# Performance work log

Hardware: AMD Instinct MI355X
Metric: run time of the kernel (lower is better)

The kernel has to match this reference:

```python
import jax, jax.numpy as jnp
import numpy as np

CHUNK = 16
GROUPS = 8
EPS = 1e-5


def setup_inputs() -> dict:
    key = jax.random.key(0)
    ks = jax.random.split(key, 8)
    B, C, H, W = 8, 1, 2048, 2048
    D_in = C * CHUNK * CHUNK  # 256
    D = 16                    # out_channels
    x = jax.random.normal(ks[0], (B, C, H, W), dtype=jnp.float32)
    s_fc = 1.0 / np.sqrt(D_in)
    fc_wr = jax.random.normal(ks[1], (D, D_in), dtype=jnp.float32) * s_fc
    fc_wi = jax.random.normal(ks[2], (D, D_in), dtype=jnp.float32) * s_fc
    fc_br = jax.random.normal(ks[3], (D,), dtype=jnp.float32) * s_fc
    fc_bi = jax.random.normal(ks[4], (D,), dtype=jnp.float32) * s_fc
    conv_w = jax.random.normal(ks[5], (D, D), dtype=jnp.float32) * (1.0 / np.sqrt(D))
    conv_b = jax.random.normal(ks[6], (D,), dtype=jnp.float32) * 0.05
    gamma = jnp.ones((D,), dtype=jnp.float32)
    beta = jnp.zeros((D,), dtype=jnp.float32)
    return {"x": x, "fc_wr": fc_wr, "fc_wi": fc_wi, "fc_br": fc_br,
            "fc_bi": fc_bi, "conv_w": conv_w, "conv_b": conv_b,
            "gamma": gamma, "beta": beta}


def reference(x, fc_wr, fc_wi, fc_br, fc_bi, conv_w, conv_b, gamma, beta):
    B, C, H, W = x.shape
    s = CHUNK
    h, w = H // s, W // s
    D = fc_wr.shape[0]
    # rearrange 'b c (h s1) (w s2) -> (b h w) (s1 s2 c)'
    p = x.reshape(B, C, h, s, w, s)
    p = p.transpose(0, 2, 4, 3, 5, 1).reshape(B * h * w, s * s * C)
    # FFT over the flattened patch dim (ortho norm) -> complex64
    fft = jnp.fft.fft(p, norm="ortho")
    Wc = fc_wr + 1j * fc_wi           # [D, D_in] complex
    bc = fc_br + 1j * fc_bi           # [D]
    fc = fft @ Wc.T + bc              # [N, D] complex linear
    # IFFT over channel dim (size D), keep real part
    y = jnp.fft.ifft(fc, norm="ortho").real  # [N, D] float32
    # '(b h w) d -> b d h w'
    y = y.reshape(B, h, w, D).transpose(0, 3, 1, 2)
    # 1x1 conv
    y = jnp.einsum("bdhw,ed->behw", y, conv_w) + conv_b[None, :, None, None]
    # GroupNorm(GROUPS, D)
    yg = y.reshape(B, GROUPS, D // GROUPS, h, w)
    mean = yg.mean(axis=(2, 3, 4), keepdims=True)
    var = yg.var(axis=(2, 3, 4), keepdims=True)
    yn = ((yg - mean) * jax.lax.rsqrt(var + EPS)).reshape(B, D, h, w)
    return yn * gamma[None, :, None, None] + beta[None, :, None, None]
```

## Files before the change

### kernel.cpp

```cpp
#include <hip/hip_runtime.h>
#include <math.h>

#define PI_F 3.14159265358979323846f


#define WS_AH    0
#define WS_U     2048
#define WS_STATS 2112

using half8   = __attribute__((ext_vector_type(8))) _Float16;
using floatx4 = __attribute__((ext_vector_type(4))) float;

__device__ __forceinline__ void gload_lds16(const void* g, void* l) {
    __builtin_amdgcn_global_load_lds(
        (const __attribute__((address_space(1))) uint32_t*)g,
        (__attribute__((address_space(3))) uint32_t*)l,
        16, 0, 0);
}

__global__ __launch_bounds__(256) void prep(
        const float* __restrict__ wr, const float* __restrict__ wi,
        const float* __restrict__ br, const float* __restrict__ bi,
        const float* __restrict__ cw, const float* __restrict__ cb,
        float* __restrict__ ws) {
    const int e = blockIdx.x;
    const int t = threadIdx.x;
    __shared__ float c16[16], s16[16], Fr[16], Fi[16];
    __shared__ float Gr[256], Gi[256], cosT[256], sinT[256];

    float ang = (2.0f * PI_F / 256.0f) * (float)t;
    cosT[t] = cosf(ang);
    sinT[t] = sinf(ang);
    if (t < 16) {
        float a = (2.0f * PI_F / 16.0f) * (float)t;
        c16[t] = cosf(a);
        s16[t] = sinf(a);
    }
    __syncthreads();

    if (t < 16) {
        float fr = 0.f, fi = 0.f;
        #pragma unroll
        for (int m = 0; m < 16; ++m) {
            float c = cw[e * 16 + m];
            fr += c * c16[(t * m) & 15];
            fi += c * s16[(t * m) & 15];
        }
        Fr[t] = fr;
        Fi[t] = fi;
    }
    __syncthreads();

    {
        float gr = 0.f, gi = 0.f;
        #pragma unroll
        for (int d = 0; d < 16; ++d) {
            float wrv = wr[d * 256 + t];
            float wiv = wi[d * 256 + t];
            gr += wrv * Fr[d] - wiv * Fi[d];
            gi += wrv * Fi[d] + wiv * Fr[d];
        }
        Gr[t] = gr;
        Gi[t] = gi;
    }
    if (t == 0) {
        float s = 0.f;
        #pragma unroll
        for (int d = 0; d < 16; ++d) s += br[d] * Fr[d] - bi[d] * Fi[d];
        ws[WS_U + e] = cb[e] + 0.25f * s;
    }
    __syncthreads();

    float acc = 0.f;
    for (int k = 0; k < 256; ++k) {
        int a = (k * t) & 255;
        acc += Gr[k] * cosT[a] + Gi[k] * sinT[a];
    }
    _Float16* Ah = (_Float16*)(ws + WS_AH);
    Ah[e * 256 + t] = (_Float16)(acc * (1.0f / 64.0f));

    if (e == 0 && t < 128) ws[WS_STATS + t] = 0.f;
}

__global__ __launch_bounds__(256) void main_k(const float* __restrict__ x,
                                              const float* __restrict__ ws,
                                              float* __restrict__ out,
                                              float* __restrict__ stats) {
    __shared__ float x_sh[4 * 4096];
    __shared__ float s_sum[4][8], s_ssq[4][8];
    const int t = threadIdx.x;

    const int w    = t >> 6;
    const int lane = t & 63;
    const int m    = lane & 15;
    const int kg   = lane >> 4;
    const int r_off = (kg >> 1);
    const int c_off = (kg & 1) << 3;

    const _Float16* Ah = (const _Float16*)(ws + WS_AH);
    half8 Areg[8];
    #pragma unroll
    for (int s = 0; s < 8; ++s)
        Areg[s] = *(const half8*)(Ah + m * 256 + s * 32 + kg * 8);
    const float u = ws[WS_U + m];

    const int P0  = blockIdx.x << 6;
    const int b   = P0 >> 14;
    const int pi  = P0 & 16383;
    const int ph  = pi >> 7;
    const int pw0 = pi & 127;

    const float* xb = x + ((size_t)b << 22)
                        + (size_t)(ph << 4) * 2048
                        + (size_t)((pw0 + w * 16 + m) << 4);

    float* lp = x_sh + w * 4096;
    #pragma unroll
    for (int j = 0; j < 16; ++j) {
        const int s = j >> 1, h = j & 1;
        const float* src = xb + (size_t)(2 * s + r_off) * 2048 + c_off + 4 * h;
        gload_lds16(src, lp + j * 256);
    }

    floatx4 acc = {0.f, 0.f, 0.f, 0.f};
    const float* xw = x_sh + w * 4096 + lane * 4;

#define WAITVM(N) asm volatile("s_waitcnt vmcnt(" #N ")" ::: "memory")
#define STEP(S, VM) do {                                                 \
        WAITVM(VM);                                                      \
        const float4 c0 = *(const float4*)(xw + (S) * 512);              \
        const float4 c1 = *(const float4*)(xw + (S) * 512 + 256);        \
        half8 a;                                                         \
        a[0] = (_Float16)c0.x; a[1] = (_Float16)c0.y;                    \
        a[2] = (_Float16)c0.z; a[3] = (_Float16)c0.w;                    \
        a[4] = (_Float16)c1.x; a[5] = (_Float16)c1.y;                    \
        a[6] = (_Float16)c1.z; a[7] = (_Float16)c1.w;                    \
        acc = __builtin_amdgcn_mfma_f32_16x16x32_f16(a, Areg[S], acc,    \
                                                     0, 0, 0);           \
    } while (0)

    STEP(0, 14);
    STEP(1, 12);
    STEP(2, 10);
    STEP(3, 8);
    STEP(4, 6);
    STEP(5, 4);
    STEP(6, 2);
    STEP(7, 0);
#undef STEP
#undef WAITVM

    float v0 = acc[0] + u;
    float v1 = acc[1] + u;
    float v2 = acc[2] + u;
    float v3 = acc[3] + u;
    *(float4*)&out[((size_t)b << 18) + (size_t)m * 16384
                   + (size_t)(ph << 7) + (size_t)(pw0 + w * 16 + kg * 4)]
        = make_float4(v0, v1, v2, v3);

    float sv = v0 + v1 + v2 + v3;
    float qv = v0 * v0 + v1 * v1 + v2 * v2 + v3 * v3;
    sv += __shfl_xor(sv, 16, 64);  qv += __shfl_xor(qv, 16, 64);
    sv += __shfl_xor(sv, 32, 64);  qv += __shfl_xor(qv, 32, 64);
    sv += __shfl_xor(sv, 1, 64);   qv += __shfl_xor(qv, 1, 64);
    if (kg == 0 && (m & 1) == 0) {
        s_sum[w][m >> 1] = sv;
        s_ssq[w][m >> 1] = qv;
    }
    __syncthreads();
    if (t < 8) {
        float S = s_sum[0][t] + s_sum[1][t] + s_sum[2][t] + s_sum[3][t];
        float Q = s_ssq[0][t] + s_ssq[1][t] + s_ssq[2][t] + s_ssq[3][t];
        atomicAdd(&stats[b * 8 + t],      S);
        atomicAdd(&stats[64 + b * 8 + t], Q);
    }
}

__global__ __launch_bounds__(256) void finalize(float* __restrict__ out,
                                                const float* __restrict__ stats,
                                                const float* __restrict__ gamma,
                                                const float* __restrict__ beta) {
    const int i    = blockIdx.x * 256 + threadIdx.x;
    const int flat = i << 2;
    const int b = flat >> 18;
    const int c = (flat >> 14) & 15;
    const int g = c >> 1;

    const float inv_n = 1.0f / 32768.0f;
    float mean = stats[b * 8 + g] * inv_n;
    float var  = stats[64 + b * 8 + g] * inv_n - mean * mean;
    float rstd = rsqrtf(var + 1e-5f);
    float sc = rstd * gamma[c];
    float sh = beta[c] - mean * sc;

    float4 vv = ((float4*)out)[i];
    vv.x = vv.x * sc + sh;
    vv.y = vv.y * sc + sh;
    vv.z = vv.z * sc + sh;
    vv.w = vv.w * sc + sh;
    ((float4*)out)[i] = vv;
}

extern "C" void kernel_launch(void* const* d_in, const int* in_sizes, int n_in,
                              void* d_out, int out_size, void* d_ws, size_t ws_size,
                              hipStream_t stream) {
    const float* x  = (const float*)d_in[0];
    const float* wr = (const float*)d_in[1];
    const float* wi = (const float*)d_in[2];
    const float* br = (const float*)d_in[3];
    const float* bi = (const float*)d_in[4];
    const float* cw = (const float*)d_in[5];
    const float* cb = (const float*)d_in[6];
    const float* gm = (const float*)d_in[7];
    const float* bt = (const float*)d_in[8];
    float* out = (float*)d_out;
    float* ws  = (float*)d_ws;

    prep<<<16, 256, 0, stream>>>(wr, wi, br, bi, cw, cb, ws);
    main_k<<<2048, 256, 0, stream>>>(x, ws, out, ws + WS_STATS);
    finalize<<<2048, 256, 0, stream>>>(out, ws + WS_STATS, gm, bt);
}
```

Measured before the change: 220.2 us.

## Fuse GroupNorm finalize into main kernel via cooperative grid sync

Replaces the separate finalize pass with a cooperative launch of 512 blocks, each processing four patch tiles with double-buffered global-to-LDS loads. After the grid-wide sync the blocks read the group statistics and write normalized outputs straight from registers. This avoids writing and re-reading the full output tensor and drops one kernel launch. In exchange it relies on all 512 blocks being co-resident and adds grid-sync latency and less parallelism per block.

```diff
diff --git a/kernel.cpp b/kernel.cpp
--- a/kernel.cpp
+++ b/kernel.cpp
@@ -1,5 +1,8 @@
 #include <hip/hip_runtime.h>
+#include <hip/hip_cooperative_groups.h>
 #include <math.h>
+
+namespace cg = cooperative_groups;
 
 #define PI_F 3.14159265358979323846f
 
@@ -85,8 +88,10 @@
 __global__ __launch_bounds__(256) void main_k(const float* __restrict__ x,
                                               const float* __restrict__ ws,
                                               float* __restrict__ out,
+                                              const float* __restrict__ gamma,
+                                              const float* __restrict__ beta,
                                               float* __restrict__ stats) {
-    __shared__ float x_sh[4 * 4096];
+    __shared__ float x_sh[16384];
     __shared__ float s_sum[4][8], s_ssq[4][8];
     const int t = threadIdx.x;
 
@@ -104,62 +109,89 @@
         Areg[s] = *(const half8*)(Ah + m * 256 + s * 32 + kg * 8);
     const float u = ws[WS_U + m];
 
-    const int P0  = blockIdx.x << 6;
-    const int b   = P0 >> 14;
-    const int pi  = P0 & 16383;
-    const int ph  = pi >> 7;
-    const int pw0 = pi & 127;
-
-    const float* xb = x + ((size_t)b << 22)
-                        + (size_t)(ph << 4) * 2048
-                        + (size_t)((pw0 + w * 16 + m) << 4);
-
-    float* lp = x_sh + w * 4096;
-    #pragma unroll
-    for (int j = 0; j < 16; ++j) {
-        const int s = j >> 1, h = j & 1;
-        const float* src = xb + (size_t)(2 * s + r_off) * 2048 + c_off + 4 * h;
-        gload_lds16(src, lp + j * 256);
-    }
-
+    const int T0  = blockIdx.x << 2;
+    const int b   = T0 >> 8;
+    const int tb0 = T0 & 255;
+    const int ph01 = tb0 >> 1;
+    const int cl   = (w * 16 + m) << 4;
+
+    const float* xB  = x + ((size_t)b << 22);
+    const float* xbA = xB + (size_t)(ph01 << 4) * 2048 + cl;
+    const float* xbB = xbA + 1024;
+    const float* xbC = xbA + 32768;
+    const float* xbD = xbC + 1024;
+
+#define ISSUE(G, XB) do {                                                  \
+        float* lp_ = x_sh + ((G) & 1) * 8192 + w * 2048;                   \
+        _Pragma("unroll")                                                  \
+        for (int j = 0; j < 8; ++j) {                                      \
+            const int sg_ = ((G) & 1) * 4 + (j >> 1);                      \
+            const float* src_ = (XB) + (size_t)(2 * sg_ + r_off) * 2048    \
+                                + c_off + 4 * (j & 1);                     \
+            gload_lds16(src_, lp_ + j * 256);                              \
+        }                                                                  \
+    } while (0)
+
+    const float* xw0 = x_sh + w * 2048 + lane * 4;
+    const float* xw1 = xw0 + 8192;
+
+#define STEP(BUFP, SL, SG, VMLIT) do {                                     \
+        asm volatile("s_waitcnt vmcnt(" #VMLIT ")" ::: "memory");          \
+        const float4 c0 = *(const float4*)((BUFP) + (SL) * 512);           \
+        const float4 c1 = *(const float4*)((BUFP) + (SL) * 512 + 256);     \
+        half8 a;                                                           \
+        a[0] = (_Float16)c0.x; a[1] = (_Float16)c0.y;                      \
+        a[2] = (_Float16)c0.z; a[3] = (_Float16)c0.w;                      \
+        a[4] = (_Float16)c1.x; a[5] = (_Float16)c1.y;                      \
+        a[6] = (_Float16)c1.z; a[7] = (_Float16)c1.w;                      \
+        acc = __builtin_amdgcn_mfma_f32_16x16x32_f16(a, Areg[SG], acc,     \
+                                                     0, 0, 0);             \
+    } while (0)
+
+#define CONSUME_LO(P)  STEP(P,0,0,14); STEP(P,1,1,12); STEP(P,2,2,10); STEP(P,3,3,8)
+#define CONSUME_HI(P)  STEP(P,0,4,14); STEP(P,1,5,12); STEP(P,2,6,10); STEP(P,3,7,8)
+#define CONSUME_HI_LAST(P) STEP(P,0,4,6); STEP(P,1,5,4); STEP(P,2,6,2); STEP(P,3,7,0)
+
+    float4 vtA, vtB, vtC, vtD;
+    float sv = 0.f, qv = 0.f;
+#define FINISH_TILE(VT) do {                                               \
+        (VT) = make_float4(acc[0] + u, acc[1] + u, acc[2] + u, acc[3] + u);\
+        sv += (VT).x + (VT).y + (VT).z + (VT).w;                           \
+        qv += (VT).x * (VT).x + (VT).y * (VT).y                            \
+            + (VT).z * (VT).z + (VT).w * (VT).w;                           \
+    } while (0)
+
+    ISSUE(0, xbA); ISSUE(1, xbA);
     floatx4 acc = {0.f, 0.f, 0.f, 0.f};
-    const float* xw = x_sh + w * 4096 + lane * 4;
-
-#define WAITVM(N) asm volatile("s_waitcnt vmcnt(" #N ")" ::: "memory")
-#define STEP(S, VM) do {                                                 \
-        WAITVM(VM);                                                      \
-        const float4 c0 = *(const float4*)(xw + (S) * 512);              \
-        const float4 c1 = *(const float4*)(xw + (S) * 512 + 256);        \
-        half8 a;                                                         \
-        a[0] = (_Float16)c0.x; a[1] = (_Float16)c0.y;                    \
-        a[2] = (_Float16)c0.z; a[3] = (_Float16)c0.w;                    \
-        a[4] = (_Float16)c1.x; a[5] = (_Float16)c1.y;                    \
-        a[6] = (_Float16)c1.z; a[7] = (_Float16)c1.w;                    \
-        acc = __builtin_amdgcn_mfma_f32_16x16x32_f16(a, Areg[S], acc,    \
-                                                     0, 0, 0);           \
-    } while (0)
-
-    STEP(0, 14);
-    STEP(1, 12);
-    STEP(2, 10);
-    STEP(3, 8);
-    STEP(4, 6);
-    STEP(5, 4);
-    STEP(6, 2);
-    STEP(7, 0);
+    CONSUME_LO(xw0);
+    ISSUE(2, xbB);
+    CONSUME_HI(xw1);
+    FINISH_TILE(vtA);
+    ISSUE(3, xbB);
+    acc = (floatx4){0.f, 0.f, 0.f, 0.f};
+    CONSUME_LO(xw0);
+    ISSUE(4, xbC);
+    CONSUME_HI(xw1);
+    FINISH_TILE(vtB);
+    ISSUE(5, xbC);
+    acc = (floatx4){0.f, 0.f, 0.f, 0.f};
+    CONSUME_LO(xw0);
+    ISSUE(6, xbD);
+    CONSUME_HI(xw1);
+    FINISH_TILE(vtC);
+    ISSUE(7, xbD);
+    acc = (floatx4){0.f, 0.f, 0.f, 0.f};
+    CONSUME_LO(xw0);
+    CONSUME_HI_LAST(xw1);
+    FINISH_TILE(vtD);
+
+#undef ISSUE
 #undef STEP
-#undef WAITVM
-
-    float v0 = acc[0] + u;
-    float v1 = acc[1] + u;
-    float v2 = acc[2] + u;
-    float v3 = acc[3] + u;
-    *(float4*)&out[((size_t)b << 18) + (size_t)m * 16384
-                   + (size_t)(ph << 7) + (size_t)(pw0 + w * 16 + kg * 4)]
-        = make_float4(v0, v1, v2, v3);
-
-    float sv = v0 + v1 + v2 + v3;
-    float qv = v0 * v0 + v1 * v1 + v2 * v2 + v3 * v3;
+#undef CONSUME_LO
+#undef CONSUME_HI
+#undef CONSUME_HI_LAST
+#undef FINISH_TILE
+
     sv += __shfl_xor(sv, 16, 64);  qv += __shfl_xor(qv, 16, 64);
     sv += __shfl_xor(sv, 32, 64);  qv += __shfl_xor(qv, 32, 64);
     sv += __shfl_xor(sv, 1, 64);   qv += __shfl_xor(qv, 1, 64);
@@ -174,31 +206,33 @@
         atomicAdd(&stats[b * 8 + t],      S);
         atomicAdd(&stats[64 + b * 8 + t], Q);
     }
-}
-
-__global__ __launch_bounds__(256) void finalize(float* __restrict__ out,
-                                                const float* __restrict__ stats,
-                                                const float* __restrict__ gamma,
-                                                const float* __restrict__ beta) {
-    const int i    = blockIdx.x * 256 + threadIdx.x;
-    const int flat = i << 2;
-    const int b = flat >> 18;
-    const int c = (flat >> 14) & 15;
-    const int g = c >> 1;
-
+
+    cg::this_grid().sync();
+
+    const int g = m >> 1;
+    float S = __hip_atomic_load(&stats[b * 8 + g],
+                                __ATOMIC_RELAXED, __HIP_MEMORY_SCOPE_AGENT);
+    float Q = __hip_atomic_load(&stats[64 + b * 8 + g],
+                                __ATOMIC_RELAXED, __HIP_MEMORY_SCOPE_AGENT);
     const float inv_n = 1.0f / 32768.0f;
-    float mean = stats[b * 8 + g] * inv_n;
-    float var  = stats[64 + b * 8 + g] * inv_n - mean * mean;
+    float mean = S * inv_n;
+    float var  = Q * inv_n - mean * mean;
     float rstd = rsqrtf(var + 1e-5f);
-    float sc = rstd * gamma[c];
-    float sh = beta[c] - mean * sc;
-
-    float4 vv = ((float4*)out)[i];
-    vv.x = vv.x * sc + sh;
-    vv.y = vv.y * sc + sh;
-    vv.z = vv.z * sc + sh;
-    vv.w = vv.w * sc + sh;
-    ((float4*)out)[i] = vv;
+    float sc = rstd * gamma[m];
+    float sh = beta[m] - mean * sc;
+
+    float* ob = out + ((size_t)b << 18) + (size_t)m * 16384
+                    + (size_t)(w * 16 + kg * 4);
+    float* oA = ob + ((size_t)ph01 << 7);
+    *(float4*)oA = make_float4(vtA.x * sc + sh, vtA.y * sc + sh,
+                               vtA.z * sc + sh, vtA.w * sc + sh);
+    *(float4*)(oA + 64) = make_float4(vtB.x * sc + sh, vtB.y * sc + sh,
+                                      vtB.z * sc + sh, vtB.w * sc + sh);
+    float* oC = oA + 128;
+    *(float4*)oC = make_float4(vtC.x * sc + sh, vtC.y * sc + sh,
+                               vtC.z * sc + sh, vtC.w * sc + sh);
+    *(float4*)(oC + 64) = make_float4(vtD.x * sc + sh, vtD.y * sc + sh,
+                                      vtD.z * sc + sh, vtD.w * sc + sh);
 }
 
 extern "C" void kernel_launch(void* const* d_in, const int* in_sizes, int n_in,
@@ -215,8 +249,12 @@
     const float* bt = (const float*)d_in[8];
     float* out = (float*)d_out;
     float* ws  = (float*)d_ws;
+    float* st  = ws + WS_STATS;
 
     prep<<<16, 256, 0, stream>>>(wr, wi, br, bi, cw, cb, ws);
-    main_k<<<2048, 256, 0, stream>>>(x, ws, out, ws + WS_STATS);
-    finalize<<<2048, 256, 0, stream>>>(out, ws + WS_STATS, gm, bt);
-}
+
+    void* args[] = {(void*)&x, (void*)&ws, (void*)&out,
+                    (void*)&gm, (void*)&bt, (void*)&st};
+    hipLaunchCooperativeKernel((const void*)main_k, dim3(512), dim3(256),
+                               args, 0, stream);
+}
```

Measured after the change: 302.7 us. 1.37x slower.

## Stage patch rows through double-buffered LDS with coalesced row loads

Applied to the files above, without the earlier changes.

Each wave now loads its 16 patches row by row, so every row fetch covers one contiguous 1KB span of global memory instead of scattered 32B pieces. The loads go into a two-stage LDS ring of 4 rows each, and the next stage is issued between MFMA steps. This halves the per-block LDS footprint, which should let more blocks stay resident per CU and overlap global loads with compute. The cost is more complex vmcnt bookkeeping and reuse of each LDS buffer within a wave. A sched_barrier pins the weight-register loads ahead of the streaming loads.

```diff
diff --git a/kernel.cpp b/kernel.cpp
--- a/kernel.cpp
+++ b/kernel.cpp
@@ -86,7 +86,7 @@
                                               const float* __restrict__ ws,
                                               float* __restrict__ out,
                                               float* __restrict__ stats) {
-    __shared__ float x_sh[4 * 4096];
+    __shared__ float x_sh[8192];
     __shared__ float s_sum[4][8], s_ssq[4][8];
     const int t = threadIdx.x;
 
@@ -94,8 +94,6 @@
     const int lane = t & 63;
     const int m    = lane & 15;
     const int kg   = lane >> 4;
-    const int r_off = (kg >> 1);
-    const int c_off = (kg & 1) << 3;
 
     const _Float16* Ah = (const _Float16*)(ws + WS_AH);
     half8 Areg[8];
@@ -103,6 +101,7 @@
     for (int s = 0; s < 8; ++s)
         Areg[s] = *(const half8*)(Ah + m * 256 + s * 32 + kg * 8);
     const float u = ws[WS_U + m];
+    __builtin_amdgcn_sched_barrier(0);
 
     const int P0  = blockIdx.x << 6;
     const int b   = P0 >> 14;
@@ -110,45 +109,53 @@
     const int ph  = pi >> 7;
     const int pw0 = pi & 127;
 
-    const float* xb = x + ((size_t)b << 22)
-                        + (size_t)(ph << 4) * 2048
-                        + (size_t)((pw0 + w * 16 + m) << 4);
-
-    float* lp = x_sh + w * 4096;
-    #pragma unroll
-    for (int j = 0; j < 16; ++j) {
-        const int s = j >> 1, h = j & 1;
-        const float* src = xb + (size_t)(2 * s + r_off) * 2048 + c_off + 4 * h;
-        gload_lds16(src, lp + j * 256);
-    }
+    const float* xw_g = x + ((size_t)b << 22)
+                          + (size_t)(ph << 4) * 2048
+                          + (size_t)((pw0 + w * 16) << 4);
+    const int src_off = (lane & 15) * 16 + (lane >> 4) * 4;
+
+    float* lw = x_sh + w * 2048;
+
+#define ISSUE4(G) do {                                                     \
+        _Pragma("unroll")                                                  \
+        for (int j = 0; j < 4; ++j) {                                      \
+            const int r_ = 4 * (G) + j;                                    \
+            gload_lds16(xw_g + (size_t)r_ * 2048 + src_off,                \
+                        lw + ((G) & 1) * 1024 + j * 256);                  \
+        }                                                                  \
+    } while (0)
+
+    const float* rb = lw + (kg >> 1) * 256 + ((kg & 1) * 2) * 64 + m * 4;
 
     floatx4 acc = {0.f, 0.f, 0.f, 0.f};
-    const float* xw = x_sh + w * 4096 + lane * 4;
-
-#define WAITVM(N) asm volatile("s_waitcnt vmcnt(" #N ")" ::: "memory")
-#define STEP(S, VM) do {                                                 \
-        WAITVM(VM);                                                      \
-        const float4 c0 = *(const float4*)(xw + (S) * 512);              \
-        const float4 c1 = *(const float4*)(xw + (S) * 512 + 256);        \
-        half8 a;                                                         \
-        a[0] = (_Float16)c0.x; a[1] = (_Float16)c0.y;                    \
-        a[2] = (_Float16)c0.z; a[3] = (_Float16)c0.w;                    \
-        a[4] = (_Float16)c1.x; a[5] = (_Float16)c1.y;                    \
-        a[6] = (_Float16)c1.z; a[7] = (_Float16)c1.w;                    \
-        acc = __builtin_amdgcn_mfma_f32_16x16x32_f16(a, Areg[S], acc,    \
-                                                     0, 0, 0);           \
+#define STEP(S, VMLIT) do {                                                \
+        asm volatile("s_waitcnt vmcnt(" #VMLIT ")" ::: "memory");          \
+        const float* p_ = rb + (((S) >> 1) & 1) * 1024 + ((S) & 1) * 512;  \
+        const float4 c0 = *(const float4*)p_;                              \
+        const float4 c1 = *(const float4*)(p_ + 64);                       \
+        half8 a;                                                           \
+        a[0] = (_Float16)c0.x; a[1] = (_Float16)c0.y;                      \
+        a[2] = (_Float16)c0.z; a[3] = (_Float16)c0.w;                      \
+        a[4] = (_Float16)c1.x; a[5] = (_Float16)c1.y;                      \
+        a[6] = (_Float16)c1.z; a[7] = (_Float16)c1.w;                      \
+        acc = __builtin_amdgcn_mfma_f32_16x16x32_f16(a, Areg[S], acc,      \
+                                                     0, 0, 0);             \
     } while (0)
 
-    STEP(0, 14);
-    STEP(1, 12);
-    STEP(2, 10);
-    STEP(3, 8);
+    ISSUE4(0);
+    ISSUE4(1);
+    STEP(0, 6);
+    STEP(1, 4);
+    ISSUE4(2);
+    STEP(2, 6);
+    STEP(3, 4);
+    ISSUE4(3);
     STEP(4, 6);
     STEP(5, 4);
     STEP(6, 2);
     STEP(7, 0);
+#undef ISSUE4
 #undef STEP
-#undef WAITVM
 
     float v0 = acc[0] + u;
     float v1 = acc[1] + u;
```

Measured after the change: 221.6 us. About the same (+0.6%).
